# Optimization experiments

Measured on AMD Instinct MI355X. Metric: run time of the kernel, lower is better.

Reference implementation:

```python
import jax, jax.numpy as jnp
import numpy as np

N, E = 50000, 800000
IN, HID, HEADS, EDIM, OUT = 128, 32, 4, 16, 1
W = HID * HEADS  # 128, encoder width


def _glorot(key, shape):
    fan_in = shape[0]
    return jax.random.normal(key, shape, dtype=jnp.float32) / np.sqrt(fan_in)


def setup_inputs() -> dict:
    key = jax.random.key(0)
    ks = jax.random.split(key, 24)
    inp = {
        "x": jax.random.normal(ks[0], (N, IN), dtype=jnp.float32),
        "edge_index": jax.random.randint(ks[1], (2, E), 0, N, dtype=jnp.int64),
        "edge_attr": jax.random.normal(ks[2], (E, EDIM), dtype=jnp.float32),
        # layer 0 (in_channels -> heads*hidden)
        "Wl0": _glorot(ks[3], (IN, W)), "bl0": jnp.zeros((W,), jnp.float32),
        "Wr0": _glorot(ks[4], (IN, W)), "br0": jnp.zeros((W,), jnp.float32),
        "We0": _glorot(ks[5], (EDIM, W)),
        "att0": _glorot(ks[6], (HEADS, HID)),
        "b0": jnp.zeros((W,), jnp.float32),
        # layer 1 (heads*hidden -> heads*hidden)
        "Wl1": _glorot(ks[7], (W, W)), "bl1": jnp.zeros((W,), jnp.float32),
        "Wr1": _glorot(ks[8], (W, W)), "br1": jnp.zeros((W,), jnp.float32),
        "We1": _glorot(ks[9], (EDIM, W)),
        "att1": _glorot(ks[10], (HEADS, HID)),
        "b1": jnp.zeros((W,), jnp.float32),
        # classifier
        "Wc": _glorot(ks[11], (W, OUT)), "bc": jnp.zeros((OUT,), jnp.float32),
    }
    return inp


def _gatv2_layer(x, src, dst, ea, Wl, bl, Wr, br, We, att, b, n_nodes):
    # GATv2Conv (PyG defaults: share_weights=False, negative_slope=0.2, concat=True)
    H, C = att.shape
    xl = (x @ Wl + bl).reshape(n_nodes, H, C)   # source-side transform
    xr = (x @ Wr + br).reshape(n_nodes, H, C)   # target-side transform
    eh = (ea @ We).reshape(-1, H, C)            # edge feature transform (no bias)
    m = xl[src] + xr[dst] + eh                  # [E', H, C] per-edge message pre-activation
    e = jnp.einsum('ehc,hc->eh', jax.nn.leaky_relu(m, 0.2), att)  # [E', H]
    # segment softmax over incoming edges of each dst node (self-loops ensure no empty segment)
    emax = jax.ops.segment_max(e, dst, num_segments=n_nodes)
    ex = jnp.exp(e - emax[dst])
    denom = jax.ops.segment_sum(ex, dst, num_segments=n_nodes)
    alpha = ex / (denom[dst] + 1e-16)
    out = jax.ops.segment_sum(alpha[..., None] * xl[src], dst, num_segments=n_nodes)
    return out.reshape(n_nodes, H * C) + b


def reference(x, edge_index, edge_attr,
              Wl0, bl0, Wr0, br0, We0, att0, b0,
              Wl1, bl1, Wr1, br1, We1, att1, b1,
              Wc, bc):
    n = x.shape[0]
    src, dst = edge_index[0], edge_index[1]
    # add_self_loops with fill_value='mean': self-loop edge_attr = mean of incoming edge_attr per node
    cnt = jax.ops.segment_sum(jnp.ones((src.shape[0],), x.dtype), dst, num_segments=n)
    loop_attr = jax.ops.segment_sum(edge_attr, dst, num_segments=n) / jnp.maximum(cnt, 1.0)[:, None]
    loop = jnp.arange(n, dtype=src.dtype)
    src_a = jnp.concatenate([src, loop])
    dst_a = jnp.concatenate([dst, loop])
    ea_a = jnp.concatenate([edge_attr, loop_attr], axis=0)

    h = jax.nn.gelu(_gatv2_layer(x, src_a, dst_a, ea_a, Wl0, bl0, Wr0, br0, We0, att0, b0, n), approximate=False)
    h = jax.nn.gelu(_gatv2_layer(h, src_a, dst_a, ea_a, Wl1, bl1, Wr1, br1, We1, att1, b1, n), approximate=False)
    logits = h @ Wc + bc  # [N, 1]  (dropout inactive in eval mode)
    return logits.squeeze(-1)
```

## Files before the change

### kernel.cpp

```cpp
#include <hip/hip_runtime.h>
#include <math.h>


static inline size_t align256(size_t x) { return (x + 255) & ~size_t(255); }

__device__ __forceinline__ int clampi(int v, int lo, int hi) {
  return v < lo ? lo : (v > hi ? hi : v);
}

__global__ void k_hist(const int* __restrict__ ei, int* __restrict__ cnt, int E, int n) {
  int i = blockIdx.x * blockDim.x + threadIdx.x;
  if (i >= E) return;
  int dst = clampi(ei[E + i], 0, n - 1);
  atomicAdd(&cnt[dst], 1);
}

__global__ void k_scan(const int* __restrict__ cnt, int* __restrict__ row_ptr, int n) {
  const int T = 1024;
  __shared__ int wsum[16], wbase[16];
  int tid = threadIdx.x;
  int chunk = (n + T - 1) / T;
  int lo = tid * chunk; if (lo > n) lo = n;
  int hi = lo + chunk;  if (hi > n) hi = n;
  int s = 0;
  for (int i = lo; i < hi; ++i) s += cnt[i] + 1;
  int lane = tid & 63, w = tid >> 6;
  int incl = s;
  #pragma unroll
  for (int d = 1; d < 64; d <<= 1) {
    int v = __shfl_up(incl, d, 64);
    if (lane >= d) incl += v;
  }
  if (lane == 63) wsum[w] = incl;
  __syncthreads();
  if (tid == 0) {
    int a = 0;
    for (int i = 0; i < 16; ++i) { wbase[i] = a; a += wsum[i]; }
  }
  __syncthreads();
  int run = wbase[w] + (incl - s);
  if (tid == 0) row_ptr[0] = 0;
  for (int i = lo; i < hi; ++i) { run += cnt[i] + 1; row_ptr[i + 1] = run; }
}

__global__ void k_scatter(const int* __restrict__ ei, int* __restrict__ cursor,
                          int2* __restrict__ col, int E, int n) {
  int i = blockIdx.x * blockDim.x + threadIdx.x;
  if (i < E) {
    int src = clampi(ei[i], 0, n - 1);
    int dst = clampi(ei[E + i], 0, n - 1);
    int pos = atomicAdd(&cursor[dst], 1);
    col[pos] = make_int2(src, i);
  } else if (i < E + n) {
    int node = i - E;
    int pos = atomicAdd(&cursor[node], 1);
    col[pos] = make_int2(node, E + node);
  }
}

__global__ void k_loop_mean(const int* __restrict__ row_ptr, const int2* __restrict__ col,
                            const float* __restrict__ ea, float* __restrict__ lsum,
                            int n, int E) {
  int t = blockIdx.x * blockDim.x + threadIdx.x;
  if (t >= n * 16) return;
  int node = t >> 4, d = t & 15;
  int beg = row_ptr[node], end = row_ptr[node + 1];
  float s = 0.f;
  int c = 0;
  for (int i = beg; i < end; ++i) {
    int2 se = col[i];
    if (se.y < E) { s += ea[(size_t)se.y * 16 + d]; ++c; }
  }
  lsum[t] = s / (float)(c > 0 ? c : 1);
}

__launch_bounds__(256)
__global__ void k_transform(const float* __restrict__ in, const float* __restrict__ Wl,
                            const float* __restrict__ bl, const float* __restrict__ Wr,
                            const float* __restrict__ br, float* __restrict__ xl,
                            float* __restrict__ xr, int n) {
  __shared__ float As[16][128];
  int tid = threadIdx.x;
  int row0 = blockIdx.x * 16;
  int rows = n - row0; if (rows > 16) rows = 16;
  const float4* in4 = (const float4*)(in + (size_t)row0 * 128);
  float4* As4 = (float4*)As;
  for (int i = tid; i < rows * 32; i += 256) As4[i] = in4[i];
  __syncthreads();
  int c = tid;
  const float* B = (c < 128) ? Wl : Wr;
  int cc = c & 127;
  float bias = (c < 128) ? bl[cc] : br[cc];
  float acc[16];
  #pragma unroll
  for (int i = 0; i < 16; ++i) acc[i] = bias;
  for (int k = 0; k < 128; k += 4) {
    float b0 = B[(k + 0) * 128 + cc], b1 = B[(k + 1) * 128 + cc];
    float b2 = B[(k + 2) * 128 + cc], b3 = B[(k + 3) * 128 + cc];
    #pragma unroll
    for (int r = 0; r < 16; ++r) {
      float4 a = *(const float4*)&As[r][k];
      acc[r] += a.x * b0 + a.y * b1 + a.z * b2 + a.w * b3;
    }
  }
  float* op = (c < 128) ? xl : xr;
  for (int r = 0; r < rows; ++r) op[(size_t)(row0 + r) * 128 + cc] = acc[r];
}

#define EDGE_STEP(SRC, EID, MX, DEN, A0, A1)                                     \
  do {                                                                           \
    const float* ep = ((EID) < E) ? (ea + (size_t)(EID) * 16)                    \
                                  : (loop_attr + (size_t)((EID) - E) * 16);      \
    float2 xlv = *(const float2*)(xl + (size_t)(SRC) * 128 + lane * 2);          \
    float4 v0 = ((const float4*)ep)[0];                                          \
    float4 v1 = ((const float4*)ep)[1];                                          \
    float4 v2 = ((const float4*)ep)[2];                                          \
    float4 v3 = ((const float4*)ep)[3];                                          \
    float eh0 = v0.x * we0[0] + v0.y * we0[1] + v0.z * we0[2] + v0.w * we0[3];   \
    float eh1 = v0.x * we1[0] + v0.y * we1[1] + v0.z * we1[2] + v0.w * we1[3];   \
    eh0 += v1.x * we0[4] + v1.y * we0[5] + v1.z * we0[6] + v1.w * we0[7];        \
    eh1 += v1.x * we1[4] + v1.y * we1[5] + v1.z * we1[6] + v1.w * we1[7];        \
    eh0 += v2.x * we0[8] + v2.y * we0[9] + v2.z * we0[10] + v2.w * we0[11];      \
    eh1 += v2.x * we1[8] + v2.y * we1[9] + v2.z * we1[10] + v2.w * we1[11];      \
    eh0 += v3.x * we0[12] + v3.y * we0[13] + v3.z * we0[14] + v3.w * we0[15];    \
    eh1 += v3.x * we1[12] + v3.y * we1[13] + v3.z * we1[14] + v3.w * we1[15];    \
    float m0 = xlv.x + xrv.x + eh0;                                              \
    float m1 = xlv.y + xrv.y + eh1;                                              \
    float l0 = fmaxf(m0, 0.2f * m0);                        \
    float l1 = fmaxf(m1, 0.2f * m1);                                             \
    float p = l0 * att0 + l1 * att1;                                             \
    p += __shfl_xor(p, 1);                                                       \
    p += __shfl_xor(p, 2);                                                       \
    p += __shfl_xor(p, 4);                                                       \
    p += __shfl_xor(p, 8);                                                       \
    float nm = fmaxf(MX, p);                                                     \
    float sc = __expf(MX - nm);                                                  \
    float w  = __expf(p - nm);                                                   \
    DEN = DEN * sc + w;                                                          \
    A0  = A0 * sc + w * xlv.x;                                                   \
    A1  = A1 * sc + w * xlv.y;                                                   \
    MX  = nm;                                                                    \
  } while (0)

__launch_bounds__(256)
__global__ void k_aggregate(const float* __restrict__ xl, const float* __restrict__ xr,
                            const int* __restrict__ row_ptr, const int2* __restrict__ col,
                            const float* __restrict__ ea, const float* __restrict__ loop_attr,
                            const float* __restrict__ We, const float* __restrict__ att,
                            const float* __restrict__ bvec, float* __restrict__ out,
                            int n, int E) {
  int wv = threadIdx.x >> 6, lane = threadIdx.x & 63;
  int node = blockIdx.x * 4 + wv;
  if (node >= n) return;
  int c0 = lane * 2, c1 = lane * 2 + 1;
  float we0[16], we1[16];
  #pragma unroll
  for (int d = 0; d < 16; ++d) {
    we0[d] = We[d * 128 + c0];
    we1[d] = We[d * 128 + c1];
  }
  float att0 = att[c0], att1 = att[c1];
  float2 xrv = *(const float2*)(xr + (size_t)node * 128 + lane * 2);
  int beg = __builtin_amdgcn_readfirstlane(row_ptr[node]);
  int end = __builtin_amdgcn_readfirstlane(row_ptr[node + 1]);
  float mA = -INFINITY, dA = 0.f, a0A = 0.f, a1A = 0.f;
  float mB = -INFINITY, dB = 0.f, a0B = 0.f, a1B = 0.f;
  int i = beg;
  #pragma unroll 2
  for (; i + 1 < end; i += 2) {
    int2 sa = col[i];
    int2 sb = col[i + 1];
    int srcA = __builtin_amdgcn_readfirstlane(sa.x);
    int eidA = __builtin_amdgcn_readfirstlane(sa.y);
    int srcB = __builtin_amdgcn_readfirstlane(sb.x);
    int eidB = __builtin_amdgcn_readfirstlane(sb.y);
    EDGE_STEP(srcA, eidA, mA, dA, a0A, a1A);
    EDGE_STEP(srcB, eidB, mB, dB, a0B, a1B);
  }
  if (i < end) {
    int2 sa = col[i];
    int srcA = __builtin_amdgcn_readfirstlane(sa.x);
    int eidA = __builtin_amdgcn_readfirstlane(sa.y);
    EDGE_STEP(srcA, eidA, mA, dA, a0A, a1A);
  }
  float nm = fmaxf(mA, mB);
  float eA = __expf(mA - nm), eB = __expf(mB - nm);
  float den  = dA * eA + dB * eB;
  float acc0 = a0A * eA + a0B * eB;
  float acc1 = a1A * eA + a1B * eB;
  float inv = 1.f / (den + 1e-16f);
  float2 bv = ((const float2*)bvec)[lane];
  float o0 = acc0 * inv + bv.x;
  float o1 = acc1 * inv + bv.y;
  o0 = 0.5f * o0 * (1.f + erff(o0 * 0.70710678118654752f));
  o1 = 0.5f * o1 * (1.f + erff(o1 * 0.70710678118654752f));
  *(float2*)(out + (size_t)node * 128 + lane * 2) = make_float2(o0, o1);
}

__global__ void k_classifier(const float* __restrict__ h, const float* __restrict__ Wc,
                             const float* __restrict__ bc, float* __restrict__ out, int n) {
  int node = blockIdx.x * blockDim.x + threadIdx.x;
  if (node >= n) return;
  const float4* hp = (const float4*)(h + (size_t)node * 128);
  const float4* wp = (const float4*)Wc;
  float acc = 0.f;
  #pragma unroll
  for (int k = 0; k < 32; ++k) {
    float4 a = hp[k];
    float4 w = wp[k];
    acc += a.x * w.x + a.y * w.y + a.z * w.z + a.w * w.w;
  }
  out[node] = acc + bc[0];
}

extern "C" void kernel_launch(void* const* d_in, const int* in_sizes, int n_in,
                              void* d_out, int out_size, void* d_ws, size_t ws_size,
                              hipStream_t stream) {
  const float* x    = (const float*)d_in[0];
  const int*   ei   = (const int*)d_in[1];
  const float* ea   = (const float*)d_in[2];
  const float* Wl0  = (const float*)d_in[3];
  const float* bl0  = (const float*)d_in[4];
  const float* Wr0  = (const float*)d_in[5];
  const float* br0  = (const float*)d_in[6];
  const float* We0  = (const float*)d_in[7];
  const float* att0 = (const float*)d_in[8];
  const float* b0   = (const float*)d_in[9];
  const float* Wl1  = (const float*)d_in[10];
  const float* bl1  = (const float*)d_in[11];
  const float* Wr1  = (const float*)d_in[12];
  const float* br1  = (const float*)d_in[13];
  const float* We1  = (const float*)d_in[14];
  const float* att1 = (const float*)d_in[15];
  const float* b1   = (const float*)d_in[16];
  const float* Wc   = (const float*)d_in[17];
  const float* bc   = (const float*)d_in[18];
  float* out = (float*)d_out;

  int n  = in_sizes[0] / 128;
  int E  = in_sizes[1] / 2;
  int Ep = E + n;

  char* ws = (char*)d_ws;
  size_t off = 0;
  auto alloc = [&](size_t bytes) { size_t o = off; off = align256(off + bytes); return o; };
  int*   cnt     = (int*)  (ws + alloc((size_t)n * 4));
  float* lsum    = (float*)(ws + alloc((size_t)n * 16 * 4));
  int*   row_ptr = (int*)  (ws + alloc((size_t)(n + 1) * 4));
  int*   cursor  = (int*)  (ws + alloc((size_t)n * 4));
  int2*  col     = (int2*) (ws + alloc((size_t)Ep * 8));
  float* xl      = (float*)(ws + alloc((size_t)n * 128 * 4));
  float* xr      = (float*)(ws + alloc((size_t)n * 128 * 4));
  float* hbuf    = (float*)(ws + alloc((size_t)n * 128 * 4));
  (void)ws_size; (void)n_in; (void)out_size;

  hipMemsetAsync(cnt, 0, (size_t)n * 4, stream);
  k_hist<<<(E + 255) / 256, 256, 0, stream>>>(ei, cnt, E, n);
  k_scan<<<1, 1024, 0, stream>>>(cnt, row_ptr, n);
  hipMemcpyAsync(cursor, row_ptr, (size_t)n * 4, hipMemcpyDeviceToDevice, stream);
  k_scatter<<<(Ep + 255) / 256, 256, 0, stream>>>(ei, cursor, col, E, n);
  k_loop_mean<<<(n * 16 + 255) / 256, 256, 0, stream>>>(row_ptr, col, ea, lsum, n, E);

  k_transform<<<(n + 15) / 16, 256, 0, stream>>>(x, Wl0, bl0, Wr0, br0, xl, xr, n);
  k_aggregate<<<(n + 3) / 4, 256, 0, stream>>>(xl, xr, row_ptr, col, ea, lsum,
                                               We0, att0, b0, hbuf, n, E);
  k_transform<<<(n + 15) / 16, 256, 0, stream>>>(hbuf, Wl1, bl1, Wr1, br1, xl, xr, n);
  k_aggregate<<<(n + 3) / 4, 256, 0, stream>>>(xl, xr, row_ptr, col, ea, lsum,
                                               We1, att1, b1, hbuf, n, E);
  k_classifier<<<(n + 255) / 256, 256, 0, stream>>>(hbuf, Wc, bc, out, n);
}
```

Baseline: 821.0 us.

## Parallelize CSR scan, prefetch neighbor rows, fuse classifier into last aggregate

Replaces the single-block serial prefix scan with a three-kernel multi-block scan that also writes the scatter cursor directly, removing the device-to-device copy. The aggregate loop now software-pipelines the gathers of the next two neighbors' xl rows ahead of the current edge computation to hide gather latency. The final classifier is folded into the second aggregate via a wavefront reduction, avoiding a write and re-read of the hidden buffer. This adds register pressure and two extra small launches for the scan.

```diff
diff --git a/kernel.cpp b/kernel.cpp
--- a/kernel.cpp
+++ b/kernel.cpp
@@ -15,15 +15,21 @@
   atomicAdd(&cnt[dst], 1);
 }
 
-__global__ void k_scan(const int* __restrict__ cnt, int* __restrict__ row_ptr, int n) {
-  const int T = 1024;
-  __shared__ int wsum[16], wbase[16];
+__global__ void k_scan1(const int* __restrict__ cnt, int* __restrict__ tmp,
+                        int* __restrict__ bsum, int n) {
+  __shared__ int wsum[4], wbase[4], total;
   int tid = threadIdx.x;
-  int chunk = (n + T - 1) / T;
-  int lo = tid * chunk; if (lo > n) lo = n;
-  int hi = lo + chunk;  if (hi > n) hi = n;
-  int s = 0;
-  for (int i = lo; i < hi; ++i) s += cnt[i] + 1;
+  int base = blockIdx.x * 1024 + tid * 4;
+  int v0 = 0, v1 = 0, v2 = 0, v3 = 0;
+  if (base + 3 < n) {
+    int4 c = *(const int4*)(cnt + base);
+    v0 = c.x + 1; v1 = c.y + 1; v2 = c.z + 1; v3 = c.w + 1;
+  } else {
+    if (base + 0 < n) v0 = cnt[base + 0] + 1;
+    if (base + 1 < n) v1 = cnt[base + 1] + 1;
+    if (base + 2 < n) v2 = cnt[base + 2] + 1;
+  }
+  int s = v0 + v1 + v2 + v3;
   int lane = tid & 63, w = tid >> 6;
   int incl = s;
   #pragma unroll
@@ -35,12 +41,41 @@
   __syncthreads();
   if (tid == 0) {
     int a = 0;
-    for (int i = 0; i < 16; ++i) { wbase[i] = a; a += wsum[i]; }
-  }
-  __syncthreads();
-  int run = wbase[w] + (incl - s);
-  if (tid == 0) row_ptr[0] = 0;
-  for (int i = lo; i < hi; ++i) { run += cnt[i] + 1; row_ptr[i + 1] = run; }
+    #pragma unroll
+    for (int i = 0; i < 4; ++i) { wbase[i] = a; a += wsum[i]; }
+    total = a;
+  }
+  __syncthreads();
+  int excl = wbase[w] + (incl - s);
+  int p0 = excl + v0, p1 = p0 + v1, p2 = p1 + v2, p3 = p2 + v3;
+  if (base + 0 < n) tmp[base + 0] = p0;
+  if (base + 1 < n) tmp[base + 1] = p1;
+  if (base + 2 < n) tmp[base + 2] = p2;
+  if (base + 3 < n) tmp[base + 3] = p3;
+  if (tid == 0) bsum[blockIdx.x] = total;
+}
+
+__global__ void k_scan2(int* __restrict__ bsum, int nb) {
+  __shared__ int sh[256];
+  int tid = threadIdx.x;
+  sh[tid] = (tid < nb) ? bsum[tid] : 0;
+  __syncthreads();
+  if (tid == 0) {
+    int a = 0;
+    for (int i = 0; i < nb; ++i) { int t = sh[i]; sh[i] = a; a += t; }
+  }
+  __syncthreads();
+  if (tid < nb) bsum[tid] = sh[tid];
+}
+
+__global__ void k_scan3(const int* __restrict__ tmp, const int* __restrict__ bsum,
+                        int* __restrict__ row_ptr, int* __restrict__ cursor, int n) {
+  int i = blockIdx.x * blockDim.x + threadIdx.x;
+  if (i >= n) return;
+  int v = tmp[i] + bsum[i >> 10];
+  row_ptr[i + 1] = v;
+  if (i + 1 < n) cursor[i + 1] = v;
+  if (i == 0) { row_ptr[0] = 0; cursor[0] = 0; }
 }
 
 __global__ void k_scatter(const int* __restrict__ ei, int* __restrict__ cursor,
@@ -107,11 +142,10 @@
   for (int r = 0; r < rows; ++r) op[(size_t)(row0 + r) * 128 + cc] = acc[r];
 }
 
-#define EDGE_STEP(SRC, EID, MX, DEN, A0, A1)                                     \
+#define EDGE_STEP_P(EID, XLV, MX, DEN, A0, A1)                                   \
   do {                                                                           \
     const float* ep = ((EID) < E) ? (ea + (size_t)(EID) * 16)                    \
                                   : (loop_attr + (size_t)((EID) - E) * 16);      \
-    float2 xlv = *(const float2*)(xl + (size_t)(SRC) * 128 + lane * 2);          \
     float4 v0 = ((const float4*)ep)[0];                                          \
     float4 v1 = ((const float4*)ep)[1];                                          \
     float4 v2 = ((const float4*)ep)[2];                                          \
@@ -124,8 +158,8 @@
     eh1 += v2.x * we1[8] + v2.y * we1[9] + v2.z * we1[10] + v2.w * we1[11];      \
     eh0 += v3.x * we0[12] + v3.y * we0[13] + v3.z * we0[14] + v3.w * we0[15];    \
     eh1 += v3.x * we1[12] + v3.y * we1[13] + v3.z * we1[14] + v3.w * we1[15];    \
-    float m0 = xlv.x + xrv.x + eh0;                                              \
-    float m1 = xlv.y + xrv.y + eh1;                                              \
+    float m0 = (XLV).x + xrv.x + eh0;                                            \
+    float m1 = (XLV).y + xrv.y + eh1;                                            \
     float l0 = fmaxf(m0, 0.2f * m0);                        \
     float l1 = fmaxf(m1, 0.2f * m1);                                             \
     float p = l0 * att0 + l1 * att1;                                             \
@@ -137,8 +171,8 @@
     float sc = __expf(MX - nm);                                                  \
     float w  = __expf(p - nm);                                                   \
     DEN = DEN * sc + w;                                                          \
-    A0  = A0 * sc + w * xlv.x;                                                   \
-    A1  = A1 * sc + w * xlv.y;                                                   \
+    A0  = A0 * sc + w * (XLV).x;                                                 \
+    A1  = A1 * sc + w * (XLV).y;                                                 \
     MX  = nm;                                                                    \
   } while (0)
 
@@ -147,12 +181,13 @@
                             const int* __restrict__ row_ptr, const int2* __restrict__ col,
                             const float* __restrict__ ea, const float* __restrict__ loop_attr,
                             const float* __restrict__ We, const float* __restrict__ att,
-                            const float* __restrict__ bvec, float* __restrict__ out,
+                            const float* __restrict__ bvec, float* __restrict__ outv,
+                            const float* __restrict__ Wc, const float* __restrict__ bc,
                             int n, int E) {
   int wv = threadIdx.x >> 6, lane = threadIdx.x & 63;
   int node = blockIdx.x * 4 + wv;
   if (node >= n) return;
-  int c0 = lane * 2, c1 = lane * 2 + 1;
+  int c0 = lane * 2, c1 = c0 + 1;
   float we0[16], we1[16];
   #pragma unroll
   for (int d = 0; d < 16; ++d) {
@@ -160,28 +195,46 @@
     we1[d] = We[d * 128 + c1];
   }
   float att0 = att[c0], att1 = att[c1];
-  float2 xrv = *(const float2*)(xr + (size_t)node * 128 + lane * 2);
+  float2 xrv = *(const float2*)(xr + (size_t)node * 128 + c0);
   int beg = __builtin_amdgcn_readfirstlane(row_ptr[node]);
   int end = __builtin_amdgcn_readfirstlane(row_ptr[node + 1]);
   float mA = -INFINITY, dA = 0.f, a0A = 0.f, a1A = 0.f;
   float mB = -INFINITY, dB = 0.f, a0B = 0.f, a1B = 0.f;
   int i = beg;
-  #pragma unroll 2
-  for (; i + 1 < end; i += 2) {
-    int2 sa = col[i];
-    int2 sb = col[i + 1];
-    int srcA = __builtin_amdgcn_readfirstlane(sa.x);
-    int eidA = __builtin_amdgcn_readfirstlane(sa.y);
-    int srcB = __builtin_amdgcn_readfirstlane(sb.x);
-    int eidB = __builtin_amdgcn_readfirstlane(sb.y);
-    EDGE_STEP(srcA, eidA, mA, dA, a0A, a1A);
-    EDGE_STEP(srcB, eidB, mB, dB, a0B, a1B);
+  int eida = 0, eidb = 0;
+  float2 xa = make_float2(0.f, 0.f), xb = make_float2(0.f, 0.f);
+  if (i + 1 < end) {
+    int2 ca = col[i], cb = col[i + 1];
+    int sa = __builtin_amdgcn_readfirstlane(ca.x);
+    eida   = __builtin_amdgcn_readfirstlane(ca.y);
+    int sb = __builtin_amdgcn_readfirstlane(cb.x);
+    eidb   = __builtin_amdgcn_readfirstlane(cb.y);
+    xa = *(const float2*)(xl + (size_t)sa * 128 + c0);
+    xb = *(const float2*)(xl + (size_t)sb * 128 + c0);
+  }
+  for (; i + 3 < end; i += 2) {
+    int2 cna = col[i + 2], cnb = col[i + 3];
+    int sna = __builtin_amdgcn_readfirstlane(cna.x);
+    int ena = __builtin_amdgcn_readfirstlane(cna.y);
+    int snb = __builtin_amdgcn_readfirstlane(cnb.x);
+    int enb = __builtin_amdgcn_readfirstlane(cnb.y);
+    float2 xna = *(const float2*)(xl + (size_t)sna * 128 + c0);
+    float2 xnb = *(const float2*)(xl + (size_t)snb * 128 + c0);
+    EDGE_STEP_P(eida, xa, mA, dA, a0A, a1A);
+    EDGE_STEP_P(eidb, xb, mB, dB, a0B, a1B);
+    eida = ena; eidb = enb; xa = xna; xb = xnb;
+  }
+  if (i + 1 < end) {
+    EDGE_STEP_P(eida, xa, mA, dA, a0A, a1A);
+    EDGE_STEP_P(eidb, xb, mB, dB, a0B, a1B);
+    i += 2;
   }
   if (i < end) {
-    int2 sa = col[i];
-    int srcA = __builtin_amdgcn_readfirstlane(sa.x);
-    int eidA = __builtin_amdgcn_readfirstlane(sa.y);
-    EDGE_STEP(srcA, eidA, mA, dA, a0A, a1A);
+    int2 c = col[i];
+    int s  = __builtin_amdgcn_readfirstlane(c.x);
+    int e2 = __builtin_amdgcn_readfirstlane(c.y);
+    float2 xv = *(const float2*)(xl + (size_t)s * 128 + c0);
+    EDGE_STEP_P(e2, xv, mA, dA, a0A, a1A);
   }
   float nm = fmaxf(mA, mB);
   float eA = __expf(mA - nm), eB = __expf(mB - nm);
@@ -194,23 +247,18 @@
   float o1 = acc1 * inv + bv.y;
   o0 = 0.5f * o0 * (1.f + erff(o0 * 0.70710678118654752f));
   o1 = 0.5f * o1 * (1.f + erff(o1 * 0.70710678118654752f));
-  *(float2*)(out + (size_t)node * 128 + lane * 2) = make_float2(o0, o1);
-}
-
-__global__ void k_classifier(const float* __restrict__ h, const float* __restrict__ Wc,
-                             const float* __restrict__ bc, float* __restrict__ out, int n) {
-  int node = blockIdx.x * blockDim.x + threadIdx.x;
-  if (node >= n) return;
-  const float4* hp = (const float4*)(h + (size_t)node * 128);
-  const float4* wp = (const float4*)Wc;
-  float acc = 0.f;
-  #pragma unroll
-  for (int k = 0; k < 32; ++k) {
-    float4 a = hp[k];
-    float4 w = wp[k];
-    acc += a.x * w.x + a.y * w.y + a.z * w.z + a.w * w.w;
-  }
-  out[node] = acc + bc[0];
+  if (Wc) {
+    float part = o0 * Wc[c0] + o1 * Wc[c1];
+    part += __shfl_xor(part, 1);
+    part += __shfl_xor(part, 2);
+    part += __shfl_xor(part, 4);
+    part += __shfl_xor(part, 8);
+    part += __shfl_xor(part, 16);
+    part += __shfl_xor(part, 32);
+    if (lane == 0) outv[node] = part + bc[0];
+  } else {
+    *(float2*)(outv + (size_t)node * 128 + c0) = make_float2(o0, o1);
+  }
 }
 
 extern "C" void kernel_launch(void* const* d_in, const int* in_sizes, int n_in,
@@ -240,6 +288,7 @@
   int n  = in_sizes[0] / 128;
   int E  = in_sizes[1] / 2;
   int Ep = E + n;
+  int nb = (n + 1023) / 1024;
 
   char* ws = (char*)d_ws;
   size_t off = 0;
@@ -248,6 +297,8 @@
   float* lsum    = (float*)(ws + alloc((size_t)n * 16 * 4));
   int*   row_ptr = (int*)  (ws + alloc((size_t)(n + 1) * 4));
   int*   cursor  = (int*)  (ws + alloc((size_t)n * 4));
+  int*   tmp     = (int*)  (ws + alloc((size_t)n * 4));
+  int*   bsum    = (int*)  (ws + alloc(256 * 4));
   int2*  col     = (int2*) (ws + alloc((size_t)Ep * 8));
   float* xl      = (float*)(ws + alloc((size_t)n * 128 * 4));
   float* xr      = (float*)(ws + alloc((size_t)n * 128 * 4));
@@ -256,16 +307,16 @@
 
   hipMemsetAsync(cnt, 0, (size_t)n * 4, stream);
   k_hist<<<(E + 255) / 256, 256, 0, stream>>>(ei, cnt, E, n);
-  k_scan<<<1, 1024, 0, stream>>>(cnt, row_ptr, n);
-  hipMemcpyAsync(cursor, row_ptr, (size_t)n * 4, hipMemcpyDeviceToDevice, stream);
+  k_scan1<<<nb, 256, 0, stream>>>(cnt, tmp, bsum, n);
+  k_scan2<<<1, 256, 0, stream>>>(bsum, nb);
+  k_scan3<<<(n + 255) / 256, 256, 0, stream>>>(tmp, bsum, row_ptr, cursor, n);
   k_scatter<<<(Ep + 255) / 256, 256, 0, stream>>>(ei, cursor, col, E, n);
   k_loop_mean<<<(n * 16 + 255) / 256, 256, 0, stream>>>(row_ptr, col, ea, lsum, n, E);
 
   k_transform<<<(n + 15) / 16, 256, 0, stream>>>(x, Wl0, bl0, Wr0, br0, xl, xr, n);
   k_aggregate<<<(n + 3) / 4, 256, 0, stream>>>(xl, xr, row_ptr, col, ea, lsum,
-                                               We0, att0, b0, hbuf, n, E);
+                                               We0, att0, b0, hbuf, nullptr, nullptr, n, E);
   k_transform<<<(n + 15) / 16, 256, 0, stream>>>(hbuf, Wl1, bl1, Wr1, br1, xl, xr, n);
   k_aggregate<<<(n + 3) / 4, 256, 0, stream>>>(xl, xr, row_ptr, col, ea, lsum,
-                                               We1, att1, b1, hbuf, n, E);
-  k_classifier<<<(n + 255) / 256, 256, 0, stream>>>(hbuf, Wc, bc, out, n);
-}
+                                               We1, att1, b1, out, Wc, bc, n, E);
+}
```

Result: faster. 763.7 us (-7.0%).
